# Optimization experiments

Measured on AMD Instinct MI355X. Metric: run time of the kernel, lower is better.

## Reference

```python
import jax, jax.numpy as jnp
import numpy as np

N_NODES = 100000
HIDDEN = 64
N_REL = 9
N_LAYERS = 3
N_EDGES = 1000000


def setup_inputs() -> dict:
    key = jax.random.key(0)
    k1, k2, k3, k4, k5 = jax.random.split(key, 5)
    edge_index = jax.random.randint(k1, (2, N_EDGES), 0, N_NODES, dtype=jnp.int64)
    edge_type = jax.random.randint(k2, (N_EDGES,), 0, N_REL, dtype=jnp.int64)
    embeddings = jax.random.uniform(k3, (N_NODES, HIDDEN), dtype=jnp.float32)
    weights = jax.random.uniform(k4, (N_LAYERS, 2 * N_REL, HIDDEN, HIDDEN), dtype=jnp.float32)
    biases = jax.random.uniform(k5, (N_LAYERS, 2 * N_REL, HIDDEN), dtype=jnp.float32)
    return {"edge_index": edge_index, "edge_type": edge_type,
            "embeddings": embeddings, "weights": weights, "biases": biases}


def reference(edge_index, edge_type, embeddings, weights, biases):
    # Faithful translation of RGCNEncoder.forward.
    # NOTE (faithful to source): get_messages always reads self.embeddings,
    # and both `sources` and `dests` are edge_index[d][edge_type == r].
    N, E = embeddings.shape
    L = weights.shape[0]
    R = weights.shape[1] // 2
    idx0 = edge_index[0]          # indices for direction d=0 (source == dest)
    idx1 = edge_index[1]          # indices for direction d=1
    rel0 = edge_type              # weight row r + R*0
    rel1 = edge_type + R          # weight row r + R*1

    output = embeddings
    for l in range(L):
        # Transform every node under every (relation, direction) weight once,
        # then gather per edge. Equivalent to per-relation gather->matmul, but
        # avoids materializing per-edge [E,E] weight matrices.
        T = jnp.einsum('ne,reo->rno', embeddings, weights[l])   # [2R, N, E]
        m0 = T[rel0, idx0] + biases[l][rel0]                    # [n_edges, E]
        m1 = T[rel1, idx1] + biases[l][rel1]                    # [n_edges, E]
        m = jnp.concatenate([m0, m1], axis=0)
        d = jnp.concatenate([idx0, idx1], axis=0)
        # scatter_mean over destination nodes (0 for nodes with no messages)
        s = jax.ops.segment_sum(m, d, num_segments=N)
        cnt = jax.ops.segment_sum(jnp.ones((d.shape[0],), m.dtype), d, num_segments=N)
        hidden = jnp.where(cnt[:, None] > 0, s / jnp.maximum(cnt, 1.0)[:, None], 0.0)
        if l + 1 < L:
            hidden = jax.nn.relu(hidden)
        output = hidden
    return output
```

## Files before the change

### kernel.cpp

```cpp
#include <hip/hip_runtime.h>


typedef float  floatx4 __attribute__((ext_vector_type(4)));
typedef short  shortx8 __attribute__((ext_vector_type(8)));
typedef unsigned int uint;
typedef unsigned char uchar;

#define MFMA_BF16(A, B, C) __builtin_amdgcn_mfma_f32_16x16x32_bf16((A), (B), (C), 0, 0, 0)

#define NBUF 512
#define NBKT 512
#define CAP  48

static __device__ __forceinline__ ushort f32_to_bf16_rne(float f) {
    union { float f; unsigned u; } v; v.f = f;
    unsigned r = v.u + 0x7fffu + ((v.u >> 16) & 1u);
    return (ushort)(r >> 16);
}

__global__ void rgcn_prep(const float* __restrict__ w2,
                          const float* __restrict__ b2,
                          ushort* __restrict__ wt_sw,
                          ushort* __restrict__ bias_sw) {
    int i = blockIdx.x * 256 + threadIdx.x;
    const int WELEMS = 18 * 8 * 64 * 8;
    if (i < WELEMS) {
        int r    = i >> 12;
        int rem  = i & 4095;
        int cid  = rem >> 9;
        int lane = (rem >> 3) & 63;
        int j    = i & 7;
        int nt = cid >> 1, kh = cid & 1;
        int o = nt * 16 + (lane & 15);
        int k = kh * 32 + (lane >> 4) * 8 + j;
        wt_sw[i] = f32_to_bf16_rne(w2[(r << 12) + (k << 6) + o]);
    } else {
        int i2 = i - WELEMS;
        if (i2 < 2048) {
            int nt   = i2 >> 9;
            int lane = (i2 >> 3) & 63;
            int j    = i2 & 7;
            int o  = nt * 16 + (lane & 15);
            int rr = (lane >> 4) * 8 + j;
            bias_sw[i2] = (rr < 18) ? f32_to_bf16_rne(b2[rr * 64 + o]) : (ushort)0;
        }
    }
}

__global__ __launch_bounds__(256) void rgcn_scatter(
    const int* __restrict__ ei,
    const int* __restrict__ et,
    ushort*    __restrict__ cnt_tab,
    ushort*    __restrict__ data,
    int E, int N)
{
    __shared__ uint   cur[NBKT];
    __shared__ ushort bins[NBKT][CAP];
    const int t = threadIdx.x;
    #pragma unroll
    for (int b = t; b < NBKT; b += 256) cur[b] = 0;
    __syncthreads();

    const int epb = (E + NBUF - 1) / NBUF;
    const int e0 = blockIdx.x * epb;
    const int e1 = (e0 + epb < E) ? e0 + epb : E;

    for (int e = e0 + t; e < e1; e += 256) {
        int r = et[e]; int i0 = ei[e]; int i1 = ei[E + e];
        if ((unsigned)r < 9u) {
            if ((unsigned)i0 < (unsigned)N) {
                int b = i0 >> 8;
                uint o = atomicAdd(&cur[b], 1u);
                if (o < CAP) bins[b][o] = (ushort)((i0 & 255) * 18 + r);
            }
            if ((unsigned)i1 < (unsigned)N) {
                int b = i1 >> 8;
                uint o = atomicAdd(&cur[b], 1u);
                if (o < CAP) bins[b][o] = (ushort)((i1 & 255) * 18 + 9 + r);
            }
        }
    }
    __syncthreads();

    const int blk = blockIdx.x;
    for (int b = t; b < NBKT; b += 256) {
        uint c = cur[b];
        if (c > CAP) c = CAP;
        cnt_tab[(size_t)blk * NBKT + b] = (ushort)c;
        uint words = (c + 1) >> 1;
        uint* dst = (uint*)(data + ((size_t)b * NBUF + blk) * CAP);
        const uint* srcp = (const uint*)&bins[b][0];
        for (uint wd = 0; wd < words; wd++) dst[wd] = srcp[wd];
    }
}

__global__ __launch_bounds__(256) void rgcn_bucket(
    const ushort* __restrict__ cnt_tab,
    const ushort* __restrict__ data,
    uchar*        __restrict__ cnts8)
{
    __shared__ ushort scnt[NBUF];
    __shared__ int    cnt[4608];
    const int t = threadIdx.x;
    const int b = blockIdx.x;
    #pragma unroll
    for (int i = t; i < 4608; i += 256) cnt[i] = 0;
    #pragma unroll
    for (int w = t; w < NBUF; w += 256) scnt[w] = cnt_tab[(size_t)w * NBKT + b];
    __syncthreads();

    #pragma unroll
    for (int w = t; w < NBUF; w += 256) {
        uint c = scnt[w];
        const ushort* seg = data + ((size_t)b * NBUF + w) * CAP;
        for (uint i = 0; i < c; i++) atomicAdd(&cnt[seg[i]], 1);
    }
    __syncthreads();

    uint* dst = (uint*)(cnts8 + (size_t)b * 4608);
    #pragma unroll
    for (int i = t; i < 1152; i += 256) {
        uint v = 0;
        #pragma unroll
        for (int j = 0; j < 4; j++) {
            int c = cnt[i * 4 + j];
            if (c > 255) c = 255;
            v |= ((uint)c) << (8 * j);
        }
        dst[i] = v;
    }
}

__global__ void rgcn_count32(const int* __restrict__ ei, const int* __restrict__ et,
                             int* __restrict__ cnts, int E, int N) {
    int e = blockIdx.x * 256 + threadIdx.x;
    if (e < E) {
        int r = et[e];
        int i0 = ei[e];
        int i1 = ei[E + e];
        if ((unsigned)r < 9u) {
            if ((unsigned)i0 < (unsigned)N) atomicAdd(&cnts[i0 * 18 + r], 1);
            if ((unsigned)i1 < (unsigned)N) atomicAdd(&cnts[i1 * 18 + 9 + r], 1);
        }
    }
}
__global__ void rgcn_cvt8(const int* __restrict__ c32, uchar* __restrict__ c8, int total4) {
    int i = blockIdx.x * 256 + threadIdx.x;
    if (i < total4) {
        uint v = 0;
        #pragma unroll
        for (int j = 0; j < 4; j++) {
            int c = c32[i * 4 + j];
            if (c > 255) c = 255;
            v |= ((uint)c) << (8 * j);
        }
        ((uint*)c8)[i] = v;
    }
}

static __device__ __forceinline__ void load_af(
    const float* __restrict__ emb, int n, int q, shortx8 af[2])
{
    const float* rp = emb + (size_t)n * 64 + q * 8;
    #pragma unroll
    for (int kh = 0; kh < 2; kh++) {
        floatx4 lo = *(const floatx4*)(rp + kh * 32);
        floatx4 hi = *(const floatx4*)(rp + kh * 32 + 4);
        shortx8 f;
        #pragma unroll
        for (int j = 0; j < 4; j++) {
            f[j]     = (short)f32_to_bf16_rne(lo[j]);
            f[j + 4] = (short)f32_to_bf16_rne(hi[j]);
        }
        af[kh] = f;
    }
}

__global__ __launch_bounds__(256, 2) void rgcn_main(
    const float*  __restrict__ emb,
    const uchar*  __restrict__ cnts8,
    const ushort* __restrict__ wt_sw,
    const ushort* __restrict__ bias_sw,
    float*        __restrict__ out,
    int N)
{
    __shared__ float  wft[18][256];
    __shared__ ushort wbL[256][32];
    __shared__ uchar  craw[4608];

    const int t    = threadIdx.x;
    const int nb   = blockIdx.x * 256;
    const int wave = t >> 6;
    const int lane = t & 63;
    const int m    = lane & 15;
    const int q    = lane >> 4;
    const int rowbase = nb + wave * 64;
    const int lrow    = wave * 64;

    {
        const uint* srcp = (const uint*)(cnts8 + (size_t)blockIdx.x * 4608);
        uint* d = (uint*)craw;
        #pragma unroll
        for (int i = t; i < 1152; i += 256) d[i] = srcp[i];
    }

    shortx8 af[4][2];
    #pragma unroll
    for (int mt = 0; mt < 4; mt++) {
        int n = rowbase + mt * 16 + m;
        if (n >= N) n = N - 1;
        load_af(emb, n, q, af[mt]);
    }

    const ushort* wbase = wt_sw + (size_t)lane * 8;
    shortx8 bA[8], bB[8];
    #pragma unroll
    for (int c = 0; c < 8; c++) bA[c] = *(const shortx8*)(wbase + c * 512);

    __syncthreads();

    {
        int c[18]; int cnt = 0;
        const uchar* cp = &craw[t * 18];
        #pragma unroll
        for (int r = 0; r < 18; r++) { c[r] = cp[r]; cnt += c[r]; }
        float inv = (cnt > 0) ? (1.0f / (float)cnt) : 0.0f;
        #pragma unroll
        for (int r = 0; r < 18; r++) {
            float w = (float)c[r] * inv;
            wft[r][t] = w;
            wbL[t][r] = f32_to_bf16_rne(w);
        }
        #pragma unroll
        for (int r = 18; r < 32; r++) wbL[t][r] = 0;
    }

    __syncthreads();

    floatx4 acc[4][4];
    #pragma unroll
    for (int mt = 0; mt < 4; mt++)
        #pragma unroll
        for (int nt = 0; nt < 4; nt++)
            acc[mt][nt] = (floatx4){0.f, 0.f, 0.f, 0.f};

    for (int r = 0; r < 18; r += 2) {
        {
            const ushort* p = wbase + (size_t)(r + 1) * 4096;
            #pragma unroll
            for (int c = 0; c < 8; c++) bB[c] = *(const shortx8*)(p + c * 512);
        }
        {
            floatx4 swv[4];
            #pragma unroll
            for (int mt = 0; mt < 4; mt++)
                swv[mt] = *(const floatx4*)&wft[r][lrow + mt * 16 + q * 4];
            #pragma unroll
            for (int nt = 0; nt < 4; nt++)
                #pragma unroll
                for (int mt = 0; mt < 4; mt++) {
                    floatx4 tmp = (floatx4){0.f, 0.f, 0.f, 0.f};
                    tmp = MFMA_BF16(af[mt][0], bA[nt * 2 + 0], tmp);
                    tmp = MFMA_BF16(af[mt][1], bA[nt * 2 + 1], tmp);
                    acc[mt][nt] += swv[mt] * tmp;
                }
        }
        if (r + 2 < 18) {
            const ushort* p = wbase + (size_t)(r + 2) * 4096;
            #pragma unroll
            for (int c = 0; c < 8; c++) bA[c] = *(const shortx8*)(p + c * 512);
        }
        {
            floatx4 swv[4];
            #pragma unroll
            for (int mt = 0; mt < 4; mt++)
                swv[mt] = *(const floatx4*)&wft[r + 1][lrow + mt * 16 + q * 4];
            #pragma unroll
            for (int nt = 0; nt < 4; nt++)
                #pragma unroll
                for (int mt = 0; mt < 4; mt++) {
                    floatx4 tmp = (floatx4){0.f, 0.f, 0.f, 0.f};
                    tmp = MFMA_BF16(af[mt][0], bB[nt * 2 + 0], tmp);
                    tmp = MFMA_BF16(af[mt][1], bB[nt * 2 + 1], tmp);
                    acc[mt][nt] += swv[mt] * tmp;
                }
        }
    }

    #pragma unroll
    for (int nt = 0; nt < 4; nt++) {
        shortx8 btf = *(const shortx8*)(bias_sw + ((size_t)nt * 64 + lane) * 8);
        #pragma unroll
        for (int mt = 0; mt < 4; mt++) {
            shortx8 wfrag = *(const shortx8*)&wbL[lrow + mt * 16 + m][q * 8];
            acc[mt][nt] = MFMA_BF16(wfrag, btf, acc[mt][nt]);
        }
    }

    #pragma unroll
    for (int mt = 0; mt < 4; mt++)
        #pragma unroll
        for (int i = 0; i < 4; i++) {
            int nn = rowbase + mt * 16 + q * 4 + i;
            if (nn < N) {
                #pragma unroll
                for (int nt = 0; nt < 4; nt++)
                    out[(size_t)nn * 64 + nt * 16 + m] = acc[mt][nt][i];
            }
        }
}

extern "C" void kernel_launch(void* const* d_in, const int* in_sizes, int n_in,
                              void* d_out, int out_size, void* d_ws, size_t ws_size,
                              hipStream_t stream) {
    const int*   edge_index = (const int*)d_in[0];
    const int*   edge_type  = (const int*)d_in[1];
    const float* emb        = (const float*)d_in[2];
    const float* weights    = (const float*)d_in[3];
    const float* biases     = (const float*)d_in[4];
    float* out = (float*)d_out;

    const int E = in_sizes[1];
    const int N = in_sizes[2] / 64;
    const int nbuckets = (N + 255) >> 8;

    const float* w2 = weights + 2 * 18 * 64 * 64;
    const float* b2 = biases  + 2 * 18 * 64;

    size_t off = 0;
    auto take = [&](size_t bytes) { void* p = (char*)d_ws + off; off = (off + bytes + 63) & ~(size_t)63; return p; };
    ushort* cnt_tab = (ushort*)take((size_t)NBUF * NBKT * 2);
    ushort* data    = (ushort*)take((size_t)NBKT * NBUF * CAP * 2);
    uchar*  cnts8   = (uchar*)take((size_t)nbuckets * 4608);
    ushort* wt_sw   = (ushort*)take(73728 * 2);
    ushort* bias_sw = (ushort*)take(2048 * 2);
    size_t need = off;

    rgcn_prep<<<(73728 + 2048 + 255) / 256, 256, 0, stream>>>(w2, b2, wt_sw, bias_sw);

    if (ws_size >= need && nbuckets <= NBKT) {
        rgcn_scatter<<<NBUF, 256, 0, stream>>>(edge_index, edge_type, cnt_tab, data, E, N);
        rgcn_bucket<<<nbuckets, 256, 0, stream>>>(cnt_tab, data, cnts8);
    } else {
        int* c32 = (int*)d_ws;
        cnts8   = (uchar*)((char*)d_ws + (((size_t)nbuckets * 4608 * 4 + 63) & ~(size_t)63));
        wt_sw   = (ushort*)(cnts8 + (size_t)nbuckets * 4608);
        bias_sw = wt_sw + 73728;
        rgcn_prep<<<(73728 + 2048 + 255) / 256, 256, 0, stream>>>(w2, b2, wt_sw, bias_sw);
        hipMemsetAsync(c32, 0, (size_t)nbuckets * 4608 * 4, stream);
        rgcn_count32<<<(E + 255) / 256, 256, 0, stream>>>(edge_index, edge_type, c32, E, N);
        int total4 = nbuckets * 4608 / 4;
        rgcn_cvt8<<<(total4 + 255) / 256, 256, 0, stream>>>(c32, cnts8, total4);
    }

    rgcn_main<<<nbuckets, 256, 0, stream>>>(emb, cnts8, wt_sw, bias_sw, out, N);
}
```

Baseline: 128.7 us.

## Fuse weight prep into scatter and bucket counting into main kernel

Weight/bias prep runs as extra blocks of the scatter kernel, and the per-bucket histogram runs inside the main GEMM kernel, which builds counts in shared memory directly from the scatter bins. This cuts the pipeline from four launches to two and drops the cnts8 intermediate's global round trip. In exchange the main kernel uses more shared memory and does the atomic histogram before its GEMM, which may lower occupancy. Embedding loads are issued before the histogram so they can overlap with it.

```diff
diff --git a/kernel.cpp b/kernel.cpp
--- a/kernel.cpp
+++ b/kernel.cpp
@@ -11,6 +11,7 @@
 #define NBUF 512
 #define NBKT 512
 #define CAP  48
+#define PREP_BLOCKS 296
 
 static __device__ __forceinline__ ushort f32_to_bf16_rne(float f) {
     union { float f; unsigned u; } v; v.f = f;
@@ -18,11 +19,10 @@
     return (ushort)(r >> 16);
 }
 
-__global__ void rgcn_prep(const float* __restrict__ w2,
-                          const float* __restrict__ b2,
-                          ushort* __restrict__ wt_sw,
-                          ushort* __restrict__ bias_sw) {
-    int i = blockIdx.x * 256 + threadIdx.x;
+static __device__ __forceinline__ void prep_item(
+    int i, const float* __restrict__ w2, const float* __restrict__ b2,
+    ushort* __restrict__ wt_sw, ushort* __restrict__ bias_sw)
+{
     const int WELEMS = 18 * 8 * 64 * 8;
     if (i < WELEMS) {
         int r    = i >> 12;
@@ -47,16 +47,28 @@
     }
 }
 
-__global__ __launch_bounds__(256) void rgcn_scatter(
-    const int* __restrict__ ei,
-    const int* __restrict__ et,
-    ushort*    __restrict__ cnt_tab,
-    ushort*    __restrict__ data,
+__global__ __launch_bounds__(256) void rgcn_scatter_prep(
+    const int*   __restrict__ ei,
+    const int*   __restrict__ et,
+    const float* __restrict__ w2,
+    const float* __restrict__ b2,
+    ushort*      __restrict__ cnt_tab,
+    ushort*      __restrict__ data,
+    ushort*      __restrict__ wt_sw,
+    ushort*      __restrict__ bias_sw,
     int E, int N)
 {
     __shared__ uint   cur[NBKT];
     __shared__ ushort bins[NBKT][CAP];
+
     const int t = threadIdx.x;
+
+    if (blockIdx.x >= NBUF) {
+        int i = (blockIdx.x - NBUF) * 256 + t;
+        prep_item(i, w2, b2, wt_sw, bias_sw);
+        return;
+    }
+
     #pragma unroll
     for (int b = t; b < NBKT; b += 256) cur[b] = 0;
     __syncthreads();
@@ -94,43 +106,10 @@
     }
 }
 
-__global__ __launch_bounds__(256) void rgcn_bucket(
-    const ushort* __restrict__ cnt_tab,
-    const ushort* __restrict__ data,
-    uchar*        __restrict__ cnts8)
-{
-    __shared__ ushort scnt[NBUF];
-    __shared__ int    cnt[4608];
-    const int t = threadIdx.x;
-    const int b = blockIdx.x;
-    #pragma unroll
-    for (int i = t; i < 4608; i += 256) cnt[i] = 0;
-    #pragma unroll
-    for (int w = t; w < NBUF; w += 256) scnt[w] = cnt_tab[(size_t)w * NBKT + b];
-    __syncthreads();
-
-    #pragma unroll
-    for (int w = t; w < NBUF; w += 256) {
-        uint c = scnt[w];
-        const ushort* seg = data + ((size_t)b * NBUF + w) * CAP;
-        for (uint i = 0; i < c; i++) atomicAdd(&cnt[seg[i]], 1);
-    }
-    __syncthreads();
-
-    uint* dst = (uint*)(cnts8 + (size_t)b * 4608);
-    #pragma unroll
-    for (int i = t; i < 1152; i += 256) {
-        uint v = 0;
-        #pragma unroll
-        for (int j = 0; j < 4; j++) {
-            int c = cnt[i * 4 + j];
-            if (c > 255) c = 255;
-            v |= ((uint)c) << (8 * j);
-        }
-        dst[i] = v;
-    }
-}
-
+__global__ void rgcn_prep_k(const float* __restrict__ w2, const float* __restrict__ b2,
+                            ushort* __restrict__ wt_sw, ushort* __restrict__ bias_sw) {
+    prep_item(blockIdx.x * 256 + threadIdx.x, w2, b2, wt_sw, bias_sw);
+}
 __global__ void rgcn_count32(const int* __restrict__ ei, const int* __restrict__ et,
                              int* __restrict__ cnts, int E, int N) {
     int e = blockIdx.x * 256 + threadIdx.x;
@@ -176,66 +155,18 @@
     }
 }
 
-__global__ __launch_bounds__(256, 2) void rgcn_main(
-    const float*  __restrict__ emb,
-    const uchar*  __restrict__ cnts8,
-    const ushort* __restrict__ wt_sw,
+static __device__ __forceinline__ void gemm_store(
+    const shortx8 af[4][2],
+    const float  (*__restrict__ wft)[256],
+    const ushort (*__restrict__ wbL)[32],
+    const ushort* __restrict__ wbase,
     const ushort* __restrict__ bias_sw,
-    float*        __restrict__ out,
-    int N)
-{
-    __shared__ float  wft[18][256];
-    __shared__ ushort wbL[256][32];
-    __shared__ uchar  craw[4608];
-
-    const int t    = threadIdx.x;
-    const int nb   = blockIdx.x * 256;
-    const int wave = t >> 6;
-    const int lane = t & 63;
-    const int m    = lane & 15;
-    const int q    = lane >> 4;
-    const int rowbase = nb + wave * 64;
-    const int lrow    = wave * 64;
-
-    {
-        const uint* srcp = (const uint*)(cnts8 + (size_t)blockIdx.x * 4608);
-        uint* d = (uint*)craw;
-        #pragma unroll
-        for (int i = t; i < 1152; i += 256) d[i] = srcp[i];
-    }
-
-    shortx8 af[4][2];
-    #pragma unroll
-    for (int mt = 0; mt < 4; mt++) {
-        int n = rowbase + mt * 16 + m;
-        if (n >= N) n = N - 1;
-        load_af(emb, n, q, af[mt]);
-    }
-
-    const ushort* wbase = wt_sw + (size_t)lane * 8;
+    float* __restrict__ out, int N,
+    int lrow, int rowbase, int m, int q, int lane)
+{
     shortx8 bA[8], bB[8];
     #pragma unroll
     for (int c = 0; c < 8; c++) bA[c] = *(const shortx8*)(wbase + c * 512);
-
-    __syncthreads();
-
-    {
-        int c[18]; int cnt = 0;
-        const uchar* cp = &craw[t * 18];
-        #pragma unroll
-        for (int r = 0; r < 18; r++) { c[r] = cp[r]; cnt += c[r]; }
-        float inv = (cnt > 0) ? (1.0f / (float)cnt) : 0.0f;
-        #pragma unroll
-        for (int r = 0; r < 18; r++) {
-            float w = (float)c[r] * inv;
-            wft[r][t] = w;
-            wbL[t][r] = f32_to_bf16_rne(w);
-        }
-        #pragma unroll
-        for (int r = 18; r < 32; r++) wbL[t][r] = 0;
-    }
-
-    __syncthreads();
 
     floatx4 acc[4][4];
     #pragma unroll
@@ -308,6 +239,126 @@
                     out[(size_t)nn * 64 + nt * 16 + m] = acc[mt][nt][i];
             }
         }
+}
+
+__global__ __launch_bounds__(256, 2) void rgcn_main(
+    const float*  __restrict__ emb,
+    const ushort* __restrict__ cnt_tab,
+    const ushort* __restrict__ data,
+    const ushort* __restrict__ wt_sw,
+    const ushort* __restrict__ bias_sw,
+    float*        __restrict__ out,
+    int N)
+{
+    __shared__ int    cnt[4608];
+    __shared__ float  wft[18][256];
+    __shared__ ushort wbL[256][32];
+    __shared__ ushort scnt[NBUF];
+
+    const int t    = threadIdx.x;
+    const int b    = blockIdx.x;
+    const int wave = t >> 6;
+    const int lane = t & 63;
+    const int m    = lane & 15;
+    const int q    = lane >> 4;
+    const int rowbase = b * 256 + wave * 64;
+    const int lrow    = wave * 64;
+
+    #pragma unroll
+    for (int i = t; i < 4608; i += 256) cnt[i] = 0;
+    #pragma unroll
+    for (int w = t; w < NBUF; w += 256) scnt[w] = cnt_tab[(size_t)w * NBKT + b];
+
+    shortx8 af[4][2];
+    #pragma unroll
+    for (int mt = 0; mt < 4; mt++) {
+        int n = rowbase + mt * 16 + m;
+        if (n >= N) n = N - 1;
+        load_af(emb, n, q, af[mt]);
+    }
+    const ushort* wbase = wt_sw + (size_t)lane * 8;
+
+    __syncthreads();
+
+    #pragma unroll
+    for (int w = t; w < NBUF; w += 256) {
+        uint c = scnt[w];
+        const ushort* seg = data + ((size_t)b * NBUF + w) * CAP;
+        for (uint i = 0; i < c; i++) atomicAdd(&cnt[seg[i]], 1);
+    }
+    __syncthreads();
+
+    {
+        int c[18]; int s = 0;
+        #pragma unroll
+        for (int r = 0; r < 18; r++) { c[r] = cnt[t * 18 + r]; s += c[r]; }
+        float inv = (s > 0) ? (1.0f / (float)s) : 0.0f;
+        #pragma unroll
+        for (int r = 0; r < 18; r++) {
+            float w = (float)c[r] * inv;
+            wft[r][t] = w;
+            wbL[t][r] = f32_to_bf16_rne(w);
+        }
+        #pragma unroll
+        for (int r = 18; r < 32; r++) wbL[t][r] = 0;
+    }
+    __syncthreads();
+
+    gemm_store(af, wft, wbL, wbase, bias_sw, out, N, lrow, rowbase, m, q, lane);
+}
+
+__global__ __launch_bounds__(256, 2) void rgcn_main_c8(
+    const float*  __restrict__ emb,
+    const uchar*  __restrict__ cnts8,
+    const ushort* __restrict__ wt_sw,
+    const ushort* __restrict__ bias_sw,
+    float*        __restrict__ out,
+    int N)
+{
+    __shared__ float  wft[18][256];
+    __shared__ ushort wbL[256][32];
+    __shared__ uchar  craw[4608];
+
+    const int t    = threadIdx.x;
+    const int wave = t >> 6;
+    const int lane = t & 63;
+    const int m    = lane & 15;
+    const int q    = lane >> 4;
+    const int rowbase = blockIdx.x * 256 + wave * 64;
+    const int lrow    = wave * 64;
+
+    {
+        const uint* srcp = (const uint*)(cnts8 + (size_t)blockIdx.x * 4608);
+        uint* d = (uint*)craw;
+        #pragma unroll
+        for (int i = t; i < 1152; i += 256) d[i] = srcp[i];
+    }
+    shortx8 af[4][2];
+    #pragma unroll
+    for (int mt = 0; mt < 4; mt++) {
+        int n = rowbase + mt * 16 + m;
+        if (n >= N) n = N - 1;
+        load_af(emb, n, q, af[mt]);
+    }
+    const ushort* wbase = wt_sw + (size_t)lane * 8;
+    __syncthreads();
+    {
+        int c[18]; int s = 0;
+        const uchar* cp = &craw[t * 18];
+        #pragma unroll
+        for (int r = 0; r < 18; r++) { c[r] = cp[r]; s += c[r]; }
+        float inv = (s > 0) ? (1.0f / (float)s) : 0.0f;
+        #pragma unroll
+        for (int r = 0; r < 18; r++) {
+            float w = (float)c[r] * inv;
+            wft[r][t] = w;
+            wbL[t][r] = f32_to_bf16_rne(w);
+        }
+        #pragma unroll
+        for (int r = 18; r < 32; r++) wbL[t][r] = 0;
+    }
+    __syncthreads();
+    gemm_store(af, wft, wbL, wbase, bias_sw, out, N, lrow, rowbase, m, q, lane);
 }
 
 extern "C" void kernel_launch(void* const* d_in, const int* in_sizes, int n_in,
@@ -331,27 +382,25 @@
     auto take = [&](size_t bytes) { void* p = (char*)d_ws + off; off = (off + bytes + 63) & ~(size_t)63; return p; };
     ushort* cnt_tab = (ushort*)take((size_t)NBUF * NBKT * 2);
     ushort* data    = (ushort*)take((size_t)NBKT * NBUF * CAP * 2);
-    uchar*  cnts8   = (uchar*)take((size_t)nbuckets * 4608);
     ushort* wt_sw   = (ushort*)take(73728 * 2);
     ushort* bias_sw = (ushort*)take(2048 * 2);
     size_t need = off;
 
-    rgcn_prep<<<(73728 + 2048 + 255) / 256, 256, 0, stream>>>(w2, b2, wt_sw, bias_sw);
-
     if (ws_size >= need && nbuckets <= NBKT) {
-        rgcn_scatter<<<NBUF, 256, 0, stream>>>(edge_index, edge_type, cnt_tab, data, E, N);
-        rgcn_bucket<<<nbuckets, 256, 0, stream>>>(cnt_tab, data, cnts8);
+        rgcn_scatter_prep<<<NBUF + PREP_BLOCKS, 256, 0, stream>>>(
+            edge_index, edge_type, w2, b2, cnt_tab, data, wt_sw, bias_sw, E, N);
+        rgcn_main<<<nbuckets, 256, 0, stream>>>(
+            emb, cnt_tab, data, wt_sw, bias_sw, out, N);
     } else {
         int* c32 = (int*)d_ws;
-        cnts8   = (uchar*)((char*)d_ws + (((size_t)nbuckets * 4608 * 4 + 63) & ~(size_t)63));
+        uchar* cnts8 = (uchar*)((char*)d_ws + (((size_t)nbuckets * 4608 * 4 + 63) & ~(size_t)63));
         wt_sw   = (ushort*)(cnts8 + (size_t)nbuckets * 4608);
         bias_sw = wt_sw + 73728;
-        rgcn_prep<<<(73728 + 2048 + 255) / 256, 256, 0, stream>>>(w2, b2, wt_sw, bias_sw);
+        rgcn_prep_k<<<PREP_BLOCKS, 256, 0, stream>>>(w2, b2, wt_sw, bias_sw);
         hipMemsetAsync(c32, 0, (size_t)nbuckets * 4608 * 4, stream);
         rgcn_count32<<<(E + 255) / 256, 256, 0, stream>>>(edge_index, edge_type, c32, E, N);
         int total4 = nbuckets * 4608 / 4;
         rgcn_cvt8<<<(total4 + 255) / 256, 256, 0, stream>>>(c32, cnts8, total4);
-    }
-
-    rgcn_main<<<nbuckets, 256, 0, stream>>>(emb, cnts8, wt_sw, bias_sw, out, N);
-}
+        rgcn_main_c8<<<nbuckets, 256, 0, stream>>>(emb, cnts8, wt_sw, bias_sw, out, N);
+    }
+}
```

After: 125.2 us. 2.7% less time.
